# Kernel tuning notes

Hardware: AMD Instinct MI355X
Metric: run time of the kernel (lower is better)

## Reference

```python
import jax, jax.numpy as jnp
import numpy as np

D_MODEL = 1024
D_STATE = 16
D_CONV = 4
LN_EPS = 1e-5


def setup_inputs() -> dict:
    key = jax.random.key(0)
    ks = jax.random.split(key, 12)
    B, T, D = 2, 2048, D_MODEL
    DI, DS, K = D_MODEL, D_STATE, D_CONV
    s = lambda k, shape, fan: jax.random.normal(k, shape, dtype=jnp.float32) * (1.0 / np.sqrt(fan))
    return {
        "x": jax.random.normal(ks[0], (B, T, D), dtype=jnp.float32),
        "ln_g": jnp.ones((D,), jnp.float32),
        "ln_b": jnp.zeros((D,), jnp.float32),
        "W_in": s(ks[1], (D, 2 * DI), D),          # x @ W_in -> [B,T,2*DI]
        "conv_w": s(ks[2], (DI, 1, K), K),          # depthwise conv kernel (OIH)
        "conv_b": jnp.zeros((DI,), jnp.float32),
        "dt_w": s(ks[3], (DI, DI), DI),
        "dt_b": jnp.zeros((DI,), jnp.float32),
        "B_w": s(ks[4], (DI, DS), DI),
        "C_w": s(ks[5], (DI, DS), DI),
        "log_A": jnp.log(jnp.linspace(1.0, 16.0, DI)).astype(jnp.float32),
        "D_param": jnp.ones((DI,), jnp.float32),
        "W_out": s(ks[6], (DI, D), DI),
    }


def _layernorm(x, g, b):
    mu = jnp.mean(x, axis=-1, keepdims=True)
    var = jnp.mean(jnp.square(x - mu), axis=-1, keepdims=True)
    return (x - mu) * jax.lax.rsqrt(var + LN_EPS) * g + b


def _causal_depthwise_conv(x, w, b):
    # x: [B,T,DI], w: [DI,1,K] -> causal conv, output [B,T,DI]
    xc = jnp.transpose(x, (0, 2, 1))  # [B,DI,T]
    K = w.shape[-1]
    out = jax.lax.conv_general_dilated(
        xc, w, window_strides=(1,), padding=[(K - 1, 0)],
        dimension_numbers=("NCH", "OIH", "NCH"),
        feature_group_count=x.shape[-1])
    return jnp.transpose(out, (0, 2, 1)) + b


def _ssm_scan(x, dt, Bm, Cm, A):
    # x, dt: [B,T,DI]; Bm, Cm: [B,T,DS]; A: [DI]
    Bsz, T, DI = x.shape
    DS = Bm.shape[-1]
    h0 = jnp.zeros((Bsz, DI, DS), jnp.float32)

    def step(h, inp):
        xt, dtt, bt, ct = inp  # [B,DI],[B,DI],[B,DS],[B,DS]
        decay = jnp.exp(jnp.minimum(dtt * A, 0.0))            # [B,DI]
        h = h * decay[..., None] + (dtt * xt)[..., None] * bt[:, None, :]
        y = jnp.einsum("bds,bs->bd", h, ct)
        return h, y

    xs = (jnp.swapaxes(x, 0, 1), jnp.swapaxes(dt, 0, 1),
          jnp.swapaxes(Bm, 0, 1), jnp.swapaxes(Cm, 0, 1))
    _, ys = jax.lax.scan(step, h0, xs)  # ys: [T,B,DI]
    return jnp.swapaxes(ys, 0, 1)


def reference(x, ln_g, ln_b, W_in, conv_w, conv_b, dt_w, dt_b, B_w, C_w, log_A, D_param, W_out):
    residual = x
    xn = _layernorm(x, ln_g, ln_b)
    xz = xn @ W_in                         # [B,T,2*DI]
    x_ssm, z = jnp.split(xz, 2, axis=-1)
    x_ssm = _causal_depthwise_conv(x_ssm, conv_w, conv_b)
    x_ssm = jax.nn.silu(x_ssm)
    dt = jax.nn.softplus(x_ssm @ dt_w + dt_b)   # [B,T,DI]
    Bm = x_ssm @ B_w                            # [B,T,DS]
    Cm = x_ssm @ C_w                            # [B,T,DS]
    A = -jnp.exp(log_A.astype(jnp.float32))     # [DI]
    y = _ssm_scan(x_ssm, dt, Bm, Cm, A)
    y = y + x_ssm * D_param
    y = y * jax.nn.silu(z)
    y = y @ W_out
    return residual + y
```

## Files before the change

### kernel.cpp

```cpp
#include <hip/hip_runtime.h>
#include <cstddef>

#define TSEQ 2048
#define NB   2
#define DM   1024
#define DST  16
#define ROWS (NB*TSEQ)
#define GCH  32
#define LCH  64
#define NDTBC 1152

typedef float  f32x4  __attribute__((ext_vector_type(4)));
typedef short  bf16x8 __attribute__((ext_vector_type(8)));
typedef unsigned short us4 __attribute__((ext_vector_type(4)));
typedef unsigned short u16;

__device__ __forceinline__ float u2f(unsigned short u) {
  return __uint_as_float(((unsigned)u) << 16);
}
__device__ __forceinline__ unsigned short bf16_rn(float x) {
  unsigned u = __float_as_uint(x);
  u += 0x7fff + ((u >> 16) & 1);
  return (unsigned short)(u >> 16);
}
__device__ __forceinline__ void split1(float x, u16& h, u16& l) {
  h = bf16_rn(x);
  l = bf16_rn(x - u2f(h));
}
__device__ __forceinline__ void split4(const float4& v, us4& h, us4& l) {
  u16 h0, h1, h2, h3, l0, l1, l2, l3;
  split1(v.x, h0, l0); split1(v.y, h1, l1);
  split1(v.z, h2, l2); split1(v.w, h3, l3);
  h = (us4){h0, h1, h2, h3};
  l = (us4){l0, l1, l2, l3};
}
__device__ __forceinline__ float softplus_f(float x) {
  return fmaxf(x, 0.0f) + log1pf(expf(-fabsf(x)));
}
__device__ __forceinline__ float silu_f(float x) {
  return x / (1.0f + expf(-x));
}
__device__ __forceinline__ void async16(const void* g, void* l) {
  __builtin_amdgcn_global_load_lds(
      (const __attribute__((address_space(1))) unsigned int*)g,
      (__attribute__((address_space(3))) unsigned int*)l, 16, 0, 0);
}
__device__ __forceinline__ float block_reduce_sum(float v, float* smem) {
#pragma unroll
  for (int off = 32; off > 0; off >>= 1) v += __shfl_down(v, off);
  int wid = threadIdx.x >> 6, lane = threadIdx.x & 63;
  if (lane == 0) smem[wid] = v;
  __syncthreads();
  float r = (smem[0] + smem[1]) + (smem[2] + smem[3]);
  __syncthreads();
  return r;
}

__global__ __launch_bounds__(256) void wsplit_t(const float* __restrict__ W,
    u16* __restrict__ Th, u16* __restrict__ Tl, int K, int N) {
  __shared__ float t[32][33];
  int k0 = blockIdx.y * 32, n0 = blockIdx.x * 32;
  int r = threadIdx.x >> 3, cq = (threadIdx.x & 7) * 4;
  float4 v = *(const float4*)&W[(size_t)(k0 + r) * N + n0 + cq];
  t[r][cq + 0] = v.x; t[r][cq + 1] = v.y; t[r][cq + 2] = v.z; t[r][cq + 3] = v.w;
  __syncthreads();
  int n = threadIdx.x >> 3, kq = (threadIdx.x & 7) * 4;
  float4 w4;
  w4.x = t[kq + 0][n]; w4.y = t[kq + 1][n]; w4.z = t[kq + 2][n]; w4.w = t[kq + 3][n];
  us4 h, l;
  split4(w4, h, l);
  size_t o = (size_t)(n0 + n) * K + k0 + kq;
  *(us4*)&Th[o] = h;
  *(us4*)&Tl[o] = l;
}

__global__ __launch_bounds__(256) void bc_prep(const float* __restrict__ Bw,
    const float* __restrict__ Cw, u16* __restrict__ Th, u16* __restrict__ Tl) {
  int n = DM + blockIdx.x;
  int k = threadIdx.x * 4;
  float4 v = {0.f, 0.f, 0.f, 0.f};
  if (n < DM + DST) {
    int s = n - DM;
    v.x = Bw[(k + 0) * DST + s]; v.y = Bw[(k + 1) * DST + s];
    v.z = Bw[(k + 2) * DST + s]; v.w = Bw[(k + 3) * DST + s];
  } else if (n < DM + 2 * DST) {
    int s = n - DM - DST;
    v.x = Cw[(k + 0) * DST + s]; v.y = Cw[(k + 1) * DST + s];
    v.z = Cw[(k + 2) * DST + s]; v.w = Cw[(k + 3) * DST + s];
  }
  us4 h, l;
  split4(v, h, l);
  size_t o = (size_t)n * DM + k;
  *(us4*)&Th[o] = h;
  *(us4*)&Tl[o] = l;
}

__global__ __launch_bounds__(256) void ln_kernel(const float* __restrict__ x,
    const float* __restrict__ g, const float* __restrict__ b,
    u16* __restrict__ xh, u16* __restrict__ xl) {
  __shared__ float smem[4];
  int r = blockIdx.x;
  size_t base = (size_t)r * DM + threadIdx.x * 4;
  float4 x4 = *(const float4*)&x[base];
  float s = block_reduce_sum(x4.x + x4.y + x4.z + x4.w, smem);
  float mu = s * (1.0f / DM);
  float d0 = x4.x - mu, d1 = x4.y - mu, d2 = x4.z - mu, d3 = x4.w - mu;
  float v = block_reduce_sum(d0*d0 + d1*d1 + d2*d2 + d3*d3, smem) * (1.0f / DM);
  float inv = rsqrtf(v + 1e-5f);
  float4 g4 = *(const float4*)&g[threadIdx.x * 4];
  float4 b4 = *(const float4*)&b[threadIdx.x * 4];
  float4 o;
  o.x = d0 * inv * g4.x + b4.x;
  o.y = d1 * inv * g4.y + b4.y;
  o.z = d2 * inv * g4.z + b4.z;
  o.w = d3 * inv * g4.w + b4.w;
  us4 h, l;
  split4(o, h, l);
  *(us4*)&xh[base] = h;
  *(us4*)&xl[base] = l;
}

#define LBUF 12288
template <int EPI>
__global__ __launch_bounds__(256) void gemm_mfma(
    const u16* __restrict__ Ah, const u16* __restrict__ Al,
    const u16* __restrict__ Bh, const u16* __restrict__ Bl,
    float* __restrict__ C, int M, int N, int Kd,
    const float* __restrict__ bias, const float* __restrict__ resid,
    float* __restrict__ C2, float* __restrict__ C3) {
  __shared__ __align__(16) u16 lds[2 * LBUF];
  int tid = threadIdx.x, wave = tid >> 6, lane = tid & 63;
  int m0 = blockIdx.y * 128, n0 = blockIdx.x * 64;
  int wm = (wave >> 1) * 64, wn = (wave & 1) * 32;

  const u16* gptr[6];
  int ldst[6];
#pragma unroll
  for (int r = 0; r < 6; ++r) {
    int c = r * 256 + tid;
    int kq = c & 3;
    const u16* base;
    int row;
    if (c < 512)       { base = Ah + (size_t)m0 * Kd; row = c >> 2; }
    else if (c < 1024) { base = Al + (size_t)m0 * Kd; row = (c - 512) >> 2; }
    else if (c < 1280) { base = Bh + (size_t)n0 * Kd; row = (c - 1024) >> 2; }
    else               { base = Bl + (size_t)n0 * Kd; row = (c - 1280) >> 2; }
    gptr[r] = base + (size_t)row * Kd + kq * 8;
    ldst[r] = c * 8;
  }

  f32x4 acc[4][2];
#pragma unroll
  for (int i = 0; i < 4; ++i)
#pragma unroll
    for (int j = 0; j < 2; ++j) acc[i][j] = (f32x4){0.f, 0.f, 0.f, 0.f};
  int fr = lane & 15, quad = lane >> 4;

#pragma unroll
  for (int r = 0; r < 6; ++r) async16(gptr[r], lds + ldst[r]);

  int nsteps = Kd / 32;
  for (int s = 0; s < nsteps; ++s) {
    int cur = (s & 1) * LBUF;
    __syncthreads();
    if (s + 1 < nsteps) {
      int ko = (s + 1) * 32;
      int nxt = ((s + 1) & 1) * LBUF;
#pragma unroll
      for (int r = 0; r < 6; ++r) async16(gptr[r] + ko, lds + nxt + ldst[r]);
    }
    const u16* sAh = lds + cur;
    const u16* sAl = lds + cur + 4096;
    const u16* sBh = lds + cur + 8192;
    const u16* sBl = lds + cur + 10240;
    bf16x8 afh[4], afl[4], bfh[2], bfl[2];
#pragma unroll
    for (int t = 0; t < 4; ++t) {
      int ro = (wm + t * 16 + fr) * 32 + quad * 8;
      afh[t] = *(const bf16x8*)&sAh[ro];
      afl[t] = *(const bf16x8*)&sAl[ro];
    }
#pragma unroll
    for (int t = 0; t < 2; ++t) {
      int co = (wn + t * 16 + fr) * 32 + quad * 8;
      bfh[t] = *(const bf16x8*)&sBh[co];
      bfl[t] = *(const bf16x8*)&sBl[co];
    }
#pragma unroll
    for (int mt = 0; mt < 4; ++mt)
#pragma unroll
      for (int nt = 0; nt < 2; ++nt) {
        acc[mt][nt] = __builtin_amdgcn_mfma_f32_16x16x32_bf16(afh[mt], bfh[nt], acc[mt][nt], 0, 0, 0);
        acc[mt][nt] = __builtin_amdgcn_mfma_f32_16x16x32_bf16(afh[mt], bfl[nt], acc[mt][nt], 0, 0, 0);
        acc[mt][nt] = __builtin_amdgcn_mfma_f32_16x16x32_bf16(afl[mt], bfh[nt], acc[mt][nt], 0, 0, 0);
      }
  }

#pragma unroll
  for (int mt = 0; mt < 4; ++mt)
#pragma unroll
    for (int nt = 0; nt < 2; ++nt) {
      int col = n0 + wn + nt * 16 + fr;
#pragma unroll
      for (int r = 0; r < 4; ++r) {
        int row = m0 + wm + mt * 16 + quad * 4 + r;
        float v = acc[mt][nt][r];
        if (EPI == 2) {
          v += resid[(size_t)row * N + col];
          C[(size_t)row * N + col] = v;
        } else if (EPI == 3) {
          if (col < DM) C[(size_t)row * DM + col] = v;
          else          C2[(size_t)row * DM + col - DM] = v;
        } else if (EPI == 4) {
          if (col < DM) {
            C[(size_t)row * DM + col] = softplus_f(v + bias[col]);
          } else if (col < DM + DST) {
            C2[(size_t)row * DST + col - DM] = v;
          } else if (col < DM + 2 * DST) {
            C3[(size_t)row * DST + col - DM - DST] = v;
          }
        } else {
          C[(size_t)row * N + col] = v;
        }
      }
    }
}

__global__ __launch_bounds__(256) void conv_silu_kernel(
    const float* __restrict__ xin, const float* __restrict__ w,
    const float* __restrict__ cb, u16* __restrict__ xsh, u16* __restrict__ xsl) {
  int r = blockIdx.x;
  int b = r >> 11, t = r & 2047;
  int d = threadIdx.x * 4;
  float4 w0 = *(const float4*)&w[(d + 0) * 4];
  float4 w1 = *(const float4*)&w[(d + 1) * 4];
  float4 w2 = *(const float4*)&w[(d + 2) * 4];
  float4 w3 = *(const float4*)&w[(d + 3) * 4];
  float4 s = *(const float4*)&cb[d];
#pragma unroll
  for (int k = 0; k < 4; ++k) {
    int ts = t + k - 3;
    if (ts >= 0) {
      float4 xv = *(const float4*)&xin[((size_t)(b * TSEQ + ts)) * DM + d];
      s.x = fmaf(xv.x, (&w0.x)[k], s.x);
      s.y = fmaf(xv.y, (&w1.x)[k], s.y);
      s.z = fmaf(xv.z, (&w2.x)[k], s.z);
      s.w = fmaf(xv.w, (&w3.x)[k], s.w);
    }
  }
  float4 o;
  o.x = silu_f(s.x); o.y = silu_f(s.y); o.z = silu_f(s.z); o.w = silu_f(s.w);
  us4 h, l;
  split4(o, h, l);
  size_t base = (size_t)r * DM + d;
  *(us4*)&xsh[base] = h;
  *(us4*)&xsl[base] = l;
}

__global__ __launch_bounds__(256) void scan_pass1(
    const float* __restrict__ dt, const u16* __restrict__ xsh,
    const u16* __restrict__ xsl, const float* __restrict__ Bm,
    const float* __restrict__ logA,
    float* __restrict__ hend, float* __restrict__ pend) {
  int blk = blockIdx.x;
  int dblk = blk & 3, c = (blk >> 2) & 31, b = blk >> 7;
  int di = dblk * 256 + threadIdx.x;
  __shared__ float sB[LCH][DST];
  {
    int tl = threadIdx.x >> 2, sq = (threadIdx.x & 3) * 4;
    size_t base = ((size_t)(b * TSEQ + c * LCH + tl)) * DST + sq;
    *(float4*)&sB[tl][sq] = *(const float4*)&Bm[base];
  }
  __syncthreads();
  float A_di = -expf(logA[di]);
  float h[DST];
#pragma unroll
  for (int s = 0; s < DST; ++s) h[s] = 0.0f;
  float cp = 1.0f;
  for (int tl = 0; tl < LCH; ++tl) {
    size_t idx = ((size_t)(b * TSEQ + c * LCH + tl)) * DM + di;
    float dtv = dt[idx];
    float xv  = u2f(xsh[idx]) + u2f(xsl[idx]);
    float decay = expf(fminf(dtv * A_di, 0.0f));
    float u = dtv * xv;
#pragma unroll
    for (int s4 = 0; s4 < 4; ++s4) {
      float4 b4 = *(const float4*)&sB[tl][s4 * 4];
      h[s4*4+0] = fmaf(h[s4*4+0], decay, u * b4.x);
      h[s4*4+1] = fmaf(h[s4*4+1], decay, u * b4.y);
      h[s4*4+2] = fmaf(h[s4*4+2], decay, u * b4.z);
      h[s4*4+3] = fmaf(h[s4*4+3], decay, u * b4.w);
    }
    cp *= decay;
  }
#pragma unroll
  for (int s = 0; s < DST; ++s)
    hend[(((size_t)(b * GCH + c)) * DST + s) * DM + di] = h[s];
  pend[((size_t)(b * GCH + c)) * DM + di] = cp;
}

__global__ __launch_bounds__(256) void scan_b_kernel(
    const float* __restrict__ pend, float* __restrict__ hboth) {
  int blk = blockIdx.x;
  int dblk = blk & 3, s = (blk >> 2) & 15, b = blk >> 6;
  int di = dblk * 256 + threadIdx.x;
  float H = 0.0f;
  for (int c = 0; c < GCH; ++c) {
    size_t hidx = (((size_t)(b * GCH + c)) * DST + s) * DM + di;
    float e = hboth[hidx];
    hboth[hidx] = H;
    float P = pend[((size_t)(b * GCH + c)) * DM + di];
    H = e + P * H;
  }
}

__global__ __launch_bounds__(256) void scan_pass2(
    const float* __restrict__ dt, const u16* __restrict__ xsh,
    const u16* __restrict__ xsl, const float* __restrict__ Bm,
    const float* __restrict__ Cm, const float* __restrict__ logA,
    const float* __restrict__ Hinit, const float* __restrict__ Dp,
    const float* __restrict__ zbuf,
    u16* __restrict__ yh, u16* __restrict__ yl) {
  int blk = blockIdx.x;
  int dblk = blk & 3, c = (blk >> 2) & 31, b = blk >> 7;
  int di = dblk * 256 + threadIdx.x;
  __shared__ float sB[LCH][DST];
  __shared__ float sC[LCH][DST];
  {
    int tl = threadIdx.x >> 2, sq = (threadIdx.x & 3) * 4;
    size_t base = ((size_t)(b * TSEQ + c * LCH + tl)) * DST + sq;
    *(float4*)&sB[tl][sq] = *(const float4*)&Bm[base];
    *(float4*)&sC[tl][sq] = *(const float4*)&Cm[base];
  }
  __syncthreads();
  float A_di = -expf(logA[di]);
  float Dv = Dp[di];
  float h[DST];
  size_t hbase = ((size_t)(b * GCH + c)) * DST * DM + di;
#pragma unroll
  for (int s = 0; s < DST; ++s) h[s] = Hinit[hbase + (size_t)s * DM];
  for (int tl = 0; tl < LCH; ++tl) {
    size_t idx = ((size_t)(b * TSEQ + c * LCH + tl)) * DM + di;
    float dtv = dt[idx];
    float xv  = u2f(xsh[idx]) + u2f(xsl[idx]);
    float decay = expf(fminf(dtv * A_di, 0.0f));
    float u = dtv * xv;
    float y = 0.0f;
#pragma unroll
    for (int s4 = 0; s4 < 4; ++s4) {
      float4 b4 = *(const float4*)&sB[tl][s4 * 4];
      float4 c4 = *(const float4*)&sC[tl][s4 * 4];
      h[s4*4+0] = fmaf(h[s4*4+0], decay, u * b4.x); y = fmaf(h[s4*4+0], c4.x, y);
      h[s4*4+1] = fmaf(h[s4*4+1], decay, u * b4.y); y = fmaf(h[s4*4+1], c4.y, y);
      h[s4*4+2] = fmaf(h[s4*4+2], decay, u * b4.z); y = fmaf(h[s4*4+2], c4.z, y);
      h[s4*4+3] = fmaf(h[s4*4+3], decay, u * b4.w); y = fmaf(h[s4*4+3], c4.w, y);
    }
    y = fmaf(xv, Dv, y);
    y *= silu_f(zbuf[idx]);
    u16 hh, ll;
    split1(y, hh, ll);
    yh[idx] = hh;
    yl[idx] = ll;
  }
}

extern "C" void kernel_launch(void* const* d_in, const int* in_sizes, int n_in,
                              void* d_out, int out_size, void* d_ws, size_t ws_size,
                              hipStream_t stream) {
  const float* x      = (const float*)d_in[0];
  const float* ln_g   = (const float*)d_in[1];
  const float* ln_b   = (const float*)d_in[2];
  const float* W_in   = (const float*)d_in[3];
  const float* conv_w = (const float*)d_in[4];
  const float* conv_b = (const float*)d_in[5];
  const float* dt_w   = (const float*)d_in[6];
  const float* dt_b   = (const float*)d_in[7];
  const float* B_w    = (const float*)d_in[8];
  const float* C_w    = (const float*)d_in[9];
  const float* log_A  = (const float*)d_in[10];
  const float* D_par  = (const float*)d_in[11];
  const float* W_out  = (const float*)d_in[12];
  float* out = (float*)d_out;

  float* ws = (float*)d_ws;
  const size_t NE = (size_t)ROWS * DM;
  float* bufX  = ws;
  float* bufZ  = bufX + NE;
  float* bufW  = bufZ + NE;
  float* bufY  = bufW + NE;
  u16*   actH  = (u16*)(bufY + NE);
  u16*   actL  = actH + NE;
  float* bufDT = (float*)(actH + 2 * NE);
  u16*   yH    = (u16*)bufY;
  u16*   yL    = yH + NE;
  float* bufPe = bufW;
  u16* winTh  = (u16*)bufW;
  u16* winTl  = winTh + (size_t)2 * DM * DM;
  u16* dtbcTh = winTl + (size_t)2 * DM * DM;
  u16* dtbcTl = dtbcTh + (size_t)NDTBC * DM;
  float* bufBm = bufX;
  float* bufCm = bufBm + (size_t)ROWS * DST;
  float* bufHe = bufCm + (size_t)ROWS * DST;
  u16* woutTh  = (u16*)(bufHe + (size_t)NB * GCH * DST * DM);
  u16* woutTl  = woutTh + (size_t)DM * DM;

  wsplit_t<<<dim3(2 * DM / 32, DM / 32), 256, 0, stream>>>(W_in, winTh, winTl, DM, 2 * DM);
  wsplit_t<<<dim3(DM / 32, DM / 32), 256, 0, stream>>>(dt_w, dtbcTh, dtbcTl, DM, DM);
  bc_prep<<<NDTBC - DM, 256, 0, stream>>>(B_w, C_w, dtbcTh, dtbcTl);
  ln_kernel<<<ROWS, 256, 0, stream>>>(x, ln_g, ln_b, actH, actL);
  gemm_mfma<3><<<dim3(2 * DM / 64, ROWS / 128), 256, 0, stream>>>(
      actH, actL, winTh, winTl, bufX, ROWS, 2 * DM, DM, nullptr, nullptr, bufZ, nullptr);
  conv_silu_kernel<<<ROWS, 256, 0, stream>>>(bufX, conv_w, conv_b, actH, actL);
  wsplit_t<<<dim3(DM / 32, DM / 32), 256, 0, stream>>>(W_out, woutTh, woutTl, DM, DM);
  gemm_mfma<4><<<dim3(NDTBC / 64, ROWS / 128), 256, 0, stream>>>(
      actH, actL, dtbcTh, dtbcTl, bufDT, ROWS, NDTBC, DM, dt_b, nullptr, bufBm, bufCm);
  scan_pass1<<<NB * GCH * 4, 256, 0, stream>>>(bufDT, actH, actL, bufBm,
                                               log_A, bufHe, bufPe);
  scan_b_kernel<<<NB * DST * 4, 256, 0, stream>>>(bufPe, bufHe);
  scan_pass2<<<NB * GCH * 4, 256, 0, stream>>>(bufDT, actH, actL, bufBm, bufCm,
                                               log_A, bufHe, D_par, bufZ, yH, yL);
  gemm_mfma<2><<<dim3(DM / 64, ROWS / 128), 256, 0, stream>>>(
      yH, yL, woutTh, woutTl, out, ROWS, DM, DM, nullptr, x, nullptr, nullptr);
}
```

Measured before the change: 350.5 us.

## Retune scan chunking, trim dt/B/C padding, and add larger-tile input GEMM

The chunked scan now uses 64 chunks of 32 steps instead of 32 chunks of 64. This doubles the number of scan blocks and shortens each sequential chunk. The scan loops are unrolled, and the output dot product is split across four partial accumulators to shorten the dependency chain. The GEMM is templated on tile height and thread count: the input projection uses 256-row tiles with 512 threads, and the fused dt/B/C projection width is padded to 1088 instead of 1152. The trade-offs are a longer serial cross-chunk combine, more chunk-state memory, and higher LDS use per GEMM block, which can reduce occupancy.

```diff
diff --git a/kernel.cpp b/kernel.cpp
--- a/kernel.cpp
+++ b/kernel.cpp
@@ -6,9 +6,9 @@
 #define DM   1024
 #define DST  16
 #define ROWS (NB*TSEQ)
-#define GCH  32
-#define LCH  64
-#define NDTBC 1152
+#define GCH  64
+#define LCH  32
+#define NDTBC 1088
 
 typedef float  f32x4  __attribute__((ext_vector_type(4)));
 typedef short  bf16x8 __attribute__((ext_vector_type(8)));
@@ -120,31 +120,32 @@
   *(us4*)&xl[base] = l;
 }
 
-#define LBUF 12288
-template <int EPI>
-__global__ __launch_bounds__(256) void gemm_mfma(
+template <int EPI, int BM, int NT>
+__global__ __launch_bounds__(NT) void gemm_mfma(
     const u16* __restrict__ Ah, const u16* __restrict__ Al,
     const u16* __restrict__ Bh, const u16* __restrict__ Bl,
     float* __restrict__ C, int M, int N, int Kd,
     const float* __restrict__ bias, const float* __restrict__ resid,
     float* __restrict__ C2, float* __restrict__ C3) {
+  constexpr int LBUF = BM * 64 + 4096;
+  constexpr int ROUNDS = (BM * 8 + 512) / NT;
   __shared__ __align__(16) u16 lds[2 * LBUF];
   int tid = threadIdx.x, wave = tid >> 6, lane = tid & 63;
-  int m0 = blockIdx.y * 128, n0 = blockIdx.x * 64;
+  int m0 = blockIdx.y * BM, n0 = blockIdx.x * 64;
   int wm = (wave >> 1) * 64, wn = (wave & 1) * 32;
 
-  const u16* gptr[6];
-  int ldst[6];
-#pragma unroll
-  for (int r = 0; r < 6; ++r) {
-    int c = r * 256 + tid;
+  const u16* gptr[ROUNDS];
+  int ldst[ROUNDS];
+#pragma unroll
+  for (int r = 0; r < ROUNDS; ++r) {
+    int c = r * NT + tid;
     int kq = c & 3;
     const u16* base;
     int row;
-    if (c < 512)       { base = Ah + (size_t)m0 * Kd; row = c >> 2; }
-    else if (c < 1024) { base = Al + (size_t)m0 * Kd; row = (c - 512) >> 2; }
-    else if (c < 1280) { base = Bh + (size_t)n0 * Kd; row = (c - 1024) >> 2; }
-    else               { base = Bl + (size_t)n0 * Kd; row = (c - 1280) >> 2; }
+    if (c < BM * 4)            { base = Ah + (size_t)m0 * Kd; row = c >> 2; }
+    else if (c < BM * 8)       { base = Al + (size_t)m0 * Kd; row = (c - BM * 4) >> 2; }
+    else if (c < BM * 8 + 256) { base = Bh + (size_t)n0 * Kd; row = (c - BM * 8) >> 2; }
+    else                       { base = Bl + (size_t)n0 * Kd; row = (c - BM * 8 - 256) >> 2; }
     gptr[r] = base + (size_t)row * Kd + kq * 8;
     ldst[r] = c * 8;
   }
@@ -157,7 +158,7 @@
   int fr = lane & 15, quad = lane >> 4;
 
 #pragma unroll
-  for (int r = 0; r < 6; ++r) async16(gptr[r], lds + ldst[r]);
+  for (int r = 0; r < ROUNDS; ++r) async16(gptr[r], lds + ldst[r]);
 
   int nsteps = Kd / 32;
   for (int s = 0; s < nsteps; ++s) {
@@ -167,12 +168,12 @@
       int ko = (s + 1) * 32;
       int nxt = ((s + 1) & 1) * LBUF;
 #pragma unroll
-      for (int r = 0; r < 6; ++r) async16(gptr[r] + ko, lds + nxt + ldst[r]);
+      for (int r = 0; r < ROUNDS; ++r) async16(gptr[r] + ko, lds + nxt + ldst[r]);
     }
     const u16* sAh = lds + cur;
-    const u16* sAl = lds + cur + 4096;
-    const u16* sBh = lds + cur + 8192;
-    const u16* sBl = lds + cur + 10240;
+    const u16* sAl = lds + cur + BM * 32;
+    const u16* sBh = lds + cur + BM * 64;
+    const u16* sBl = lds + cur + BM * 64 + 2048;
     bf16x8 afh[4], afl[4], bfh[2], bfl[2];
 #pragma unroll
     for (int t = 0; t < 4; ++t) {
@@ -263,10 +264,10 @@
     const float* __restrict__ logA,
     float* __restrict__ hend, float* __restrict__ pend) {
   int blk = blockIdx.x;
-  int dblk = blk & 3, c = (blk >> 2) & 31, b = blk >> 7;
+  int dblk = blk & 3, c = (blk >> 2) & (GCH - 1), b = blk >> 8;
   int di = dblk * 256 + threadIdx.x;
   __shared__ float sB[LCH][DST];
-  {
+  if (threadIdx.x < LCH * 4) {
     int tl = threadIdx.x >> 2, sq = (threadIdx.x & 3) * 4;
     size_t base = ((size_t)(b * TSEQ + c * LCH + tl)) * DST + sq;
     *(float4*)&sB[tl][sq] = *(const float4*)&Bm[base];
@@ -277,6 +278,7 @@
 #pragma unroll
   for (int s = 0; s < DST; ++s) h[s] = 0.0f;
   float cp = 1.0f;
+#pragma unroll 4
   for (int tl = 0; tl < LCH; ++tl) {
     size_t idx = ((size_t)(b * TSEQ + c * LCH + tl)) * DM + di;
     float dtv = dt[idx];
@@ -322,14 +324,18 @@
     const float* __restrict__ zbuf,
     u16* __restrict__ yh, u16* __restrict__ yl) {
   int blk = blockIdx.x;
-  int dblk = blk & 3, c = (blk >> 2) & 31, b = blk >> 7;
+  int dblk = blk & 3, c = (blk >> 2) & (GCH - 1), b = blk >> 8;
   int di = dblk * 256 + threadIdx.x;
   __shared__ float sB[LCH][DST];
   __shared__ float sC[LCH][DST];
-  {
+  if (threadIdx.x < LCH * 4) {
     int tl = threadIdx.x >> 2, sq = (threadIdx.x & 3) * 4;
     size_t base = ((size_t)(b * TSEQ + c * LCH + tl)) * DST + sq;
     *(float4*)&sB[tl][sq] = *(const float4*)&Bm[base];
+  } else if (threadIdx.x < LCH * 8) {
+    int t2 = threadIdx.x - LCH * 4;
+    int tl = t2 >> 2, sq = (t2 & 3) * 4;
+    size_t base = ((size_t)(b * TSEQ + c * LCH + tl)) * DST + sq;
     *(float4*)&sC[tl][sq] = *(const float4*)&Cm[base];
   }
   __syncthreads();
@@ -339,22 +345,47 @@
   size_t hbase = ((size_t)(b * GCH + c)) * DST * DM + di;
 #pragma unroll
   for (int s = 0; s < DST; ++s) h[s] = Hinit[hbase + (size_t)s * DM];
+#pragma unroll 4
   for (int tl = 0; tl < LCH; ++tl) {
     size_t idx = ((size_t)(b * TSEQ + c * LCH + tl)) * DM + di;
     float dtv = dt[idx];
     float xv  = u2f(xsh[idx]) + u2f(xsl[idx]);
     float decay = expf(fminf(dtv * A_di, 0.0f));
     float u = dtv * xv;
-    float y = 0.0f;
-#pragma unroll
-    for (int s4 = 0; s4 < 4; ++s4) {
-      float4 b4 = *(const float4*)&sB[tl][s4 * 4];
-      float4 c4 = *(const float4*)&sC[tl][s4 * 4];
-      h[s4*4+0] = fmaf(h[s4*4+0], decay, u * b4.x); y = fmaf(h[s4*4+0], c4.x, y);
-      h[s4*4+1] = fmaf(h[s4*4+1], decay, u * b4.y); y = fmaf(h[s4*4+1], c4.y, y);
-      h[s4*4+2] = fmaf(h[s4*4+2], decay, u * b4.z); y = fmaf(h[s4*4+2], c4.z, y);
-      h[s4*4+3] = fmaf(h[s4*4+3], decay, u * b4.w); y = fmaf(h[s4*4+3], c4.w, y);
-    }
+    float y0 = 0.f, y1 = 0.f, y2 = 0.f, y3 = 0.f;
+    {
+      float4 b4 = *(const float4*)&sB[tl][0];
+      float4 c4 = *(const float4*)&sC[tl][0];
+      h[0] = fmaf(h[0], decay, u * b4.x); y0 = fmaf(h[0], c4.x, y0);
+      h[1] = fmaf(h[1], decay, u * b4.y); y1 = fmaf(h[1], c4.y, y1);
+      h[2] = fmaf(h[2], decay, u * b4.z); y2 = fmaf(h[2], c4.z, y2);
+      h[3] = fmaf(h[3], decay, u * b4.w); y3 = fmaf(h[3], c4.w, y3);
+    }
+    {
+      float4 b4 = *(const float4*)&sB[tl][4];
+      float4 c4 = *(const float4*)&sC[tl][4];
+      h[4] = fmaf(h[4], decay, u * b4.x); y0 = fmaf(h[4], c4.x, y0);
+      h[5] = fmaf(h[5], decay, u * b4.y); y1 = fmaf(h[5], c4.y, y1);
+      h[6] = fmaf(h[6], decay, u * b4.z); y2 = fmaf(h[6], c4.z, y2);
+      h[7] = fmaf(h[7], decay, u * b4.w); y3 = fmaf(h[7], c4.w, y3);
+    }
+    {
+      float4 b4 = *(const float4*)&sB[tl][8];
+      float4 c4 = *(const float4*)&sC[tl][8];
+      h[8]  = fmaf(h[8],  decay, u * b4.x); y0 = fmaf(h[8],  c4.x, y0);
+      h[9]  = fmaf(h[9],  decay, u * b4.y); y1 = fmaf(h[9],  c4.y, y1);
+      h[10] = fmaf(h[10], decay, u * b4.z); y2 = fmaf(h[10], c4.z, y2);
+      h[11] = fmaf(h[11], decay, u * b4.w); y3 = fmaf(h[11], c4.w, y3);
+    }
+    {
+      float4 b4 = *(const float4*)&sB[tl][12];
+      float4 c4 = *(const float4*)&sC[tl][12];
+      h[12] = fmaf(h[12], decay, u * b4.x); y0 = fmaf(h[12], c4.x, y0);
+      h[13] = fmaf(h[13], decay, u * b4.y); y1 = fmaf(h[13], c4.y, y1);
+      h[14] = fmaf(h[14], decay, u * b4.z); y2 = fmaf(h[14], c4.z, y2);
+      h[15] = fmaf(h[15], decay, u * b4.w); y3 = fmaf(h[15], c4.w, y3);
+    }
+    float y = (y0 + y1) + (y2 + y3);
     y = fmaf(xv, Dv, y);
     y *= silu_f(zbuf[idx]);
     u16 hh, ll;
@@ -408,17 +439,17 @@
   wsplit_t<<<dim3(DM / 32, DM / 32), 256, 0, stream>>>(dt_w, dtbcTh, dtbcTl, DM, DM);
   bc_prep<<<NDTBC - DM, 256, 0, stream>>>(B_w, C_w, dtbcTh, dtbcTl);
   ln_kernel<<<ROWS, 256, 0, stream>>>(x, ln_g, ln_b, actH, actL);
-  gemm_mfma<3><<<dim3(2 * DM / 64, ROWS / 128), 256, 0, stream>>>(
+  gemm_mfma<3, 256, 512><<<dim3(2 * DM / 64, ROWS / 256), 512, 0, stream>>>(
       actH, actL, winTh, winTl, bufX, ROWS, 2 * DM, DM, nullptr, nullptr, bufZ, nullptr);
   conv_silu_kernel<<<ROWS, 256, 0, stream>>>(bufX, conv_w, conv_b, actH, actL);
   wsplit_t<<<dim3(DM / 32, DM / 32), 256, 0, stream>>>(W_out, woutTh, woutTl, DM, DM);
-  gemm_mfma<4><<<dim3(NDTBC / 64, ROWS / 128), 256, 0, stream>>>(
+  gemm_mfma<4, 128, 256><<<dim3(NDTBC / 64, ROWS / 128), 256, 0, stream>>>(
       actH, actL, dtbcTh, dtbcTl, bufDT, ROWS, NDTBC, DM, dt_b, nullptr, bufBm, bufCm);
   scan_pass1<<<NB * GCH * 4, 256, 0, stream>>>(bufDT, actH, actL, bufBm,
                                                log_A, bufHe, bufPe);
   scan_b_kernel<<<NB * DST * 4, 256, 0, stream>>>(bufPe, bufHe);
   scan_pass2<<<NB * GCH * 4, 256, 0, stream>>>(bufDT, actH, actL, bufBm, bufCm,
                                                log_A, bufHe, D_par, bufZ, yH, yL);
-  gemm_mfma<2><<<dim3(DM / 64, ROWS / 128), 256, 0, stream>>>(
+  gemm_mfma<2, 128, 256><<<dim3(DM / 64, ROWS / 128), 256, 0, stream>>>(
       yH, yL, woutTh, woutTl, out, ROWS, DM, DM, nullptr, x, nullptr, nullptr);
 }
```

Measured after the change: 322.0 us. -8.1%, faster.
